# Performance work log

Measured on AMD Instinct MI355X. Metric: run time of the kernel, lower is better.

## Reference

```python
import jax, jax.numpy as jnp
import numpy as np

GEOM_W = 0.01
N_ITERS = 5
HUBER_DELTA = 1.345
LM_EPS = 1e-6


def _skew(w):
    x, y, z = w[..., 0], w[..., 1], w[..., 2]
    o = jnp.zeros_like(x)
    return jnp.stack([
        jnp.stack([o, -z, y], -1),
        jnp.stack([z, o, -x], -1),
        jnp.stack([-y, x, o], -1)], -2)


def _se3_exp(xi):
    # xi: [B,6] = (v, w), translation first (matches Jt = [I | -skew(X)])
    v, w = xi[..., :3], xi[..., 3:]
    t2 = jnp.sum(w * w, -1)[..., None, None]
    small = t2 < 1e-8
    t2s = jnp.where(small, 1.0, t2)
    th = jnp.sqrt(t2s)
    A = jnp.where(small, 1.0 - t2 / 6.0, jnp.sin(th) / th)
    Bc = jnp.where(small, 0.5 - t2 / 24.0, (1.0 - jnp.cos(th)) / t2s)
    Cc = jnp.where(small, 1.0 / 6.0 - t2 / 120.0, (th - jnp.sin(th)) / (t2s * th))
    wx = _skew(w)
    wx2 = jnp.matmul(wx, wx)
    I3 = jnp.eye(3, dtype=xi.dtype)
    R = I3 + A * wx + Bc * wx2
    V = I3 + Bc * wx + Cc * wx2
    t = jnp.einsum('bij,bj->bi', V, v)
    top = jnp.concatenate([R, t[..., None]], -1)           # [B,3,4]
    bot = jnp.broadcast_to(jnp.array([0.0, 0.0, 0.0, 1.0], dtype=xi.dtype), top[..., :1, :].shape)
    return jnp.concatenate([top, bot], -2)                 # [B,4,4]


def _grid_sample(img, gx, gy):
    # bilinear, padding_mode='zeros', align_corners=True; img [B,C,H,W], gx/gy [B,H,W] in [-1,1]
    B, C, H, W = img.shape
    x = (gx + 1.0) * 0.5 * (W - 1)
    y = (gy + 1.0) * 0.5 * (H - 1)
    x0 = jnp.floor(x)
    y0 = jnp.floor(y)
    fx1 = x - x0
    fy1 = y - y0
    flat = img.reshape(B, C, H * W)

    def corner(xi, yi, wgt):
        inb = (xi >= 0) & (xi <= W - 1) & (yi >= 0) & (yi <= H - 1)
        xc = jnp.clip(xi, 0, W - 1).astype(jnp.int32)
        yc = jnp.clip(yi, 0, H - 1).astype(jnp.int32)
        idx = (yc * W + xc).reshape(B, 1, H * W)
        vals = jnp.take_along_axis(flat, idx, axis=2).reshape(B, C, H, W)
        return vals * (wgt * inb)[:, None]

    return (corner(x0, y0, (1 - fx1) * (1 - fy1)) + corner(x0 + 1, y0, fx1 * (1 - fy1))
            + corner(x0, y0 + 1, (1 - fx1) * fy1) + corner(x0 + 1, y0 + 1, fx1 * fy1))


def _feature_gradient(img):
    # central differences with replicate padding: [B,C,H,W] -> (d/dx, d/dy)
    px = jnp.pad(img, ((0, 0), (0, 0), (0, 0), (1, 1)), mode='edge')
    py = jnp.pad(img, ((0, 0), (0, 0), (1, 1), (0, 0)), mode='edge')
    dx = 0.5 * (px[..., 2:] - px[..., :-2])
    dy = 0.5 * (py[..., 2:, :] - py[..., :-2, :])
    return dx, dy


def _forward(pose, I0, I1, invD0, invD1, intrinsics, depth0, depth1):
    B, C, H, W = I0.shape
    dt = I0.dtype
    fxv = intrinsics[:, 0][:, None, None]
    fyv = intrinsics[:, 1][:, None, None]
    cx = intrinsics[:, 2][:, None, None]
    cy = intrinsics[:, 3][:, None, None]
    vv, uu = jnp.meshgrid(jnp.arange(H, dtype=dt), jnp.arange(W, dtype=dt), indexing='ij')
    d1 = depth1[:, 0]
    # back-projected points in frame 1: [B,H,W,3]
    X1 = jnp.stack([d1 * (uu - cx) / fxv, d1 * (vv - cy) / fyv, d1], -1)
    dI0x, dI0y = _feature_gradient(I0)
    dD0x, dD0y = _feature_gradient(depth0)
    eye3 = jnp.eye(3, dtype=dt)
    lam = GEOM_W
    for _ in range(N_ITERS):
        R = pose[:, :3, :3]
        t = pose[:, :3, 3]
        X0 = jnp.einsum('bij,bhwj->bhwi', R, X1) + t[:, None, None, :]   # [B,H,W,3]
        x, y, z = X0[..., 0], X0[..., 1], X0[..., 2]
        vproj = z > 1e-6
        zs = jnp.where(vproj, z, 1.0)
        u0 = fxv * x / zs + cx
        v0 = fyv * y / zs + cy
        d = z
        inb = (u0 > 0) & (u0 < W - 1) & (v0 > 0) & (v0 < H - 1)
        valid = inb & vproj & (depth0[:, 0] > 0) & (depth1[:, 0] > 0)    # [B,H,W]
        zero = jnp.zeros_like(zs)
        row0 = jnp.stack([fxv / zs + zero, zero, -fxv * x / (zs * zs)], -1)
        row1 = jnp.stack([zero, fyv / zs + zero, -fyv * y / (zs * zs)], -1)
        Jp = jnp.stack([row0, row1], -2)                                  # [B,H,W,2,3]
        Jt = jnp.concatenate([jnp.broadcast_to(eye3, (B, H, W, 3, 3)), -_skew(X0)], -1)  # [B,H,W,3,6]
        Jw = jnp.einsum('bhwij,bhwjk->bhwik', Jp, Jt)                     # [B,H,W,2,6]
        gx = jnp.clip((u0 / (W - 1) - 0.5) * 2.0, -2.0, 2.0)
        gy = jnp.clip((v0 / (H - 1) - 0.5) * 2.0, -2.0, 2.0)
        I0w = _grid_sample(I0, gx, gy)
        r_I = I1 - I0w                                                    # [B,C,H,W]
        D0w = _grid_sample(depth0, gx, gy)
        r_Z = d[:, None] - D0w                                            # [B,1,H,W]
        gI = jnp.stack([_grid_sample(dI0x, gx, gy), _grid_sample(dI0y, gx, gy)], -1)  # [B,C,H,W,2]
        J_I = jnp.einsum('bchwn,bhwnk->bchwk', gI, Jw)                    # [B,C,H,W,6]
        gD = jnp.stack([_grid_sample(dD0x, gx, gy), _grid_sample(dD0y, gx, gy)], -1)  # [B,1,H,W,2]
        J_Z = jnp.einsum('bchwn,bhwnk->bchwk', gD, Jw) - Jt[..., 2, :][:, None]       # [B,1,H,W,6]
        vexp = jnp.broadcast_to(valid[:, None], (B, C + 1, H, W)).reshape(B, -1).astype(dt)
        J = jnp.concatenate([J_I.reshape(B, -1, 6), lam * J_Z.reshape(B, -1, 6)], 1) * vexp[..., None]
        r = jnp.concatenate([r_I.reshape(B, -1), lam * r_Z.reshape(B, -1)], 1) * vexp
        ar = jnp.abs(r)
        wts = jnp.where(ar <= HUBER_DELTA, 1.0, HUBER_DELTA / jnp.maximum(ar, 1e-8))  # Huber M-estimator
        JtJ = jnp.einsum('bnk,bnl->bkl', J, wts[..., None] * J)           # [B,6,6]
        Hs = JtJ + LM_EPS * jnp.eye(6, dtype=dt)                          # LM damping
        Rhs = jnp.einsum('bnk,bn->bk', J, wts * r)                        # [B,6]
        xi = jnp.linalg.solve(Hs, Rhs[..., None])[..., 0]                 # batched 6x6 solve
        pose = jnp.matmul(_se3_exp(xi), pose)                             # left-multiplicative retraction
    return pose


def setup_inputs() -> dict:
    key = jax.random.key(0)
    ks = jax.random.split(key, 5)
    B, C, H, W = 4, 16, 240, 320
    I0 = jax.random.normal(ks[0], (B, C, H, W), jnp.float32)
    I1 = jax.random.normal(ks[1], (B, C, H, W), jnp.float32)
    depth0 = jax.random.uniform(ks[2], (B, 1, H, W), jnp.float32, 0.5, 2.0)
    depth1 = jax.random.uniform(ks[3], (B, 1, H, W), jnp.float32, 0.5, 2.0)
    invD0 = 1.0 / depth0
    invD1 = 1.0 / depth1
    intrinsics = jnp.tile(jnp.array([[250.0, 250.0, (W - 1) / 2.0, (H - 1) / 2.0]], jnp.float32), (B, 1))
    xi0 = 0.01 * jax.random.normal(ks[4], (B, 6), jnp.float32)
    pose = _se3_exp(xi0)
    return {'pose': pose, 'I0': I0, 'I1': I1, 'invD0': invD0, 'invD1': invD1,
            'intrinsics': intrinsics, 'depth0': depth0, 'depth1': depth1}


def reference(pose, I0, I1, invD0, invD1, intrinsics, depth0, depth1):
    return _forward(pose, I0, I1, invD0, invD1, intrinsics, depth0, depth1)
```

## Files before the change

### kernel.cpp

```cpp
#include <hip/hip_runtime.h>
#include <math.h>

#define B_   4
#define C_   16
#define H_   240
#define W_   320
#define HW_  (H_*W_)
#define NPB  128
#define NBLK (HW_/NPB)
#define NACC 27
#define GEOM_W_ 0.01f
#define HUBER_  1.345f
#define LM_EPS_ 1e-6
#define N_ITERS_ 5

__global__ void dia_init(const float* __restrict__ pose_in, float* __restrict__ pose,
                         double* __restrict__ acc) {
    const int i = threadIdx.x;
    if (i < N_ITERS_ * B_ * NACC) acc[i] = 0.0;
    if (i < B_ * 16) pose[i] = pose_in[i];
}

__device__ __forceinline__ void samp12(const float* __restrict__ img,
                                       int x0, int y0, int xm1, int xp2, int ym1, int yp2,
                                       float w00, float w10, float w01, float w11,
                                       float& sv, float& sdx, float& sdy)
{
    const float* r0 = img + y0 * W_;
    const float* r1 = r0 + W_;
    float A0 = r0[xm1], A1 = r0[x0], A2 = r0[x0+1], A3 = r0[xp2];
    float B0 = r1[xm1], B1 = r1[x0], B2 = r1[x0+1], B3 = r1[xp2];
    const float* ru = img + ym1 * W_;
    const float* rd = img + yp2 * W_;
    float U0 = ru[x0], U1 = ru[x0+1];
    float D0 = rd[x0], D1 = rd[x0+1];
    sv  = w00*A1 + w10*A2 + w01*B1 + w11*B2;
    sdx = 0.5f*( w00*(A2-A0) + w10*(A3-A1) + w01*(B2-B0) + w11*(B3-B1) );
    sdy = 0.5f*( w00*(B1-U0) + w10*(B2-U1) + w01*(D0-A1) + w11*(D1-A2) );
}

__global__ __launch_bounds__(256, 6) void dia_reduce(
    const float* __restrict__ pose,
    const float* __restrict__ I0,
    const float* __restrict__ I1,
    const float* __restrict__ intr,
    const float* __restrict__ depth0,
    const float* __restrict__ depth1,
    double* __restrict__ acc)
{
    const int b    = blockIdx.y;
    const int half = threadIdx.x >> 7;
    const int lp   = threadIdx.x & 127;
    const int p    = blockIdx.x * NPB + lp;

    const float fxv = intr[b*4+0], fyv = intr[b*4+1];
    const float cx  = intr[b*4+2], cy  = intr[b*4+3];
    const float ifx = 1.0f / fxv,  ify = 1.0f / fyv;

    float Rm[9], tv[3];
#pragma unroll
    for (int i = 0; i < 3; ++i) {
#pragma unroll
        for (int j = 0; j < 3; ++j) Rm[i*3+j] = pose[b*16 + i*4 + j];
        tv[i] = pose[b*16 + i*4 + 3];
    }

    const float* d0p = depth0 + b * HW_;
    const float* d1p = depth1 + b * HW_;
    const float* I0b = I0 + (size_t)b * C_ * HW_ + (size_t)(half * 8) * HW_;
    const float* I1b = I1 + (size_t)b * C_ * HW_ + (size_t)(half * 8) * HW_;

    float c27[NACC];
#pragma unroll
    for (int i = 0; i < NACC; ++i) c27[i] = 0.f;

    {
        const int v = p / W_;
        const int u = p - v * W_;

        const float d1 = d1p[p];
        const float d0 = d0p[p];
        const float X1x = d1 * ((float)u - cx) * ifx;
        const float X1y = d1 * ((float)v - cy) * ify;
        const float x = Rm[0]*X1x + Rm[1]*X1y + Rm[2]*d1 + tv[0];
        const float y = Rm[3]*X1x + Rm[4]*X1y + Rm[5]*d1 + tv[1];
        const float z = Rm[6]*X1x + Rm[7]*X1y + Rm[8]*d1 + tv[2];

        const bool vproj = z > 1e-6f;
        const float zs = vproj ? z : 1.0f;
        const float iz = 1.0f / zs;
        const float u0 = fxv * x * iz + cx;
        const float v0 = fyv * y * iz + cy;
        const bool inb = (u0 > 0.f) && (u0 < (float)(W_-1)) && (v0 > 0.f) && (v0 < (float)(H_-1));
        const bool valid = inb && vproj && (d0 > 0.f) && (d1 > 0.f);

        if (valid) {
            const float x0f = floorf(u0), y0f = floorf(v0);
            const int x0 = (int)x0f, y0 = (int)y0f;
            const float fx1 = u0 - x0f, fy1 = v0 - y0f;
            const float w00 = (1.f-fx1)*(1.f-fy1), w10 = fx1*(1.f-fy1);
            const float w01 = (1.f-fx1)*fy1,       w11 = fx1*fy1;
            const int xm1 = max(x0-1, 0), xp2 = min(x0+2, W_-1);
            const int ym1 = max(y0-1, 0), yp2 = min(y0+2, H_-1);

            float Jw[2][6];
            {
                const float a0 = fxv * iz;
                const float a2 = -fxv * x * iz * iz;
                const float b1 = fyv * iz;
                const float b2 = -fyv * y * iz * iz;
                Jw[0][0] = a0;        Jw[0][1] = 0.f;      Jw[0][2] = a2;
                Jw[0][3] = a2 * y;    Jw[0][4] = a0*z - a2*x; Jw[0][5] = -a0*y;
                Jw[1][0] = 0.f;       Jw[1][1] = b1;       Jw[1][2] = b2;
                Jw[1][3] = -b1*z + b2*y; Jw[1][4] = -b2*x; Jw[1][5] = b1*x;
            }

            float JZ[6] = {0.f,0.f,0.f,0.f,0.f,0.f};
            float wz2 = 0.f, rZ = 0.f;
            if (half == 0) {
                float D0w, dDx, dDy;
                samp12(d0p, x0, y0, xm1, xp2, ym1, yp2, w00, w10, w01, w11, D0w, dDx, dDy);
                rZ = z - D0w;
                JZ[0] = dDx*Jw[0][0] + dDy*Jw[1][0];
                JZ[1] = dDx*Jw[0][1] + dDy*Jw[1][1];
                JZ[2] = dDx*Jw[0][2] + dDy*Jw[1][2] - 1.f;
                JZ[3] = dDx*Jw[0][3] + dDy*Jw[1][3] - y;
                JZ[4] = dDx*Jw[0][4] + dDy*Jw[1][4] + x;
                JZ[5] = dDx*Jw[0][5] + dDy*Jw[1][5];
                const float arz = fabsf(GEOM_W_ * rZ);
                const float wzw = (arz <= HUBER_) ? 1.f : HUBER_ / fmaxf(arz, 1e-8f);
                wz2 = wzw * GEOM_W_ * GEOM_W_;
            }

            float Ga = 0.f, Gb = 0.f, Gd = 0.f, grx = 0.f, gry = 0.f;
            for (int c = 0; c < 8; ++c) {
                const float* ip = I0b + c * HW_;
                float Iw, gxc, gyc;
                samp12(ip, x0, y0, xm1, xp2, ym1, yp2, w00, w10, w01, w11, Iw, gxc, gyc);
                const float r = I1b[c * HW_ + p] - Iw;
                const float ar = fabsf(r);
                const float wc = (ar <= HUBER_) ? 1.f : HUBER_ / fmaxf(ar, 1e-8f);
                Ga  += wc * gxc * gxc;
                Gb  += wc * gxc * gyc;
                Gd  += wc * gyc * gyc;
                grx += wc * r * gxc;
                gry += wc * r * gyc;
            }

            int k = 0;
#pragma unroll
            for (int i = 0; i < 6; ++i) {
#pragma unroll
                for (int j = i; j < 6; ++j) {
                    c27[k++] = Ga * Jw[0][i] * Jw[0][j]
                             + Gb * (Jw[0][i] * Jw[1][j] + Jw[1][i] * Jw[0][j])
                             + Gd * Jw[1][i] * Jw[1][j]
                             + wz2 * JZ[i] * JZ[j];
                }
            }
#pragma unroll
            for (int i = 0; i < 6; ++i)
                c27[21 + i] = grx * Jw[0][i] + gry * Jw[1][i] + wz2 * rZ * JZ[i];
        }
    }

    __shared__ float sred[4][NACC];
    const int lane = threadIdx.x & 63;
    const int wid  = threadIdx.x >> 6;
#pragma unroll
    for (int i = 0; i < NACC; ++i) {
        float vs = c27[i];
#pragma unroll
        for (int off = 32; off > 0; off >>= 1) vs += __shfl_down(vs, off, 64);
        if (lane == 0) sred[wid][i] = vs;
    }
    __syncthreads();
    if (threadIdx.x < NACC) {
        const double s = (double)sred[0][threadIdx.x] + (double)sred[1][threadIdx.x]
                       + (double)sred[2][threadIdx.x] + (double)sred[3][threadIdx.x];
        atomicAdd(&acc[b * NACC + threadIdx.x], s);
    }
}

__global__ __launch_bounds__(128) void dia_solve(const double* __restrict__ acc,
                                                 float* __restrict__ pose)
{
    __shared__ double S[B_][NACC];
    const int t = threadIdx.x;
    if (t < B_ * NACC) {
        const int b = t / NACC, i = t - b * NACC;
        S[b][i] = acc[b * NACC + i];
    }
    __syncthreads();
    if (t < B_) {
        double Hm[6][7];
        {
            double JtJ[6][6];
            int k = 0;
            for (int i = 0; i < 6; ++i)
                for (int j = i; j < 6; ++j) { JtJ[i][j] = S[t][k]; JtJ[j][i] = S[t][k]; ++k; }
            for (int i = 0; i < 6; ++i) {
                for (int j = 0; j < 6; ++j) Hm[i][j] = JtJ[i][j] + (i == j ? LM_EPS_ : 0.0);
                Hm[i][6] = S[t][21 + i];
            }
        }
        double xi[6];
        for (int col = 0; col < 6; ++col) {
            int piv = col; double mx = fabs(Hm[col][col]);
            for (int r2 = col+1; r2 < 6; ++r2) { double a = fabs(Hm[r2][col]); if (a > mx) { mx = a; piv = r2; } }
            if (piv != col)
                for (int j2 = col; j2 < 7; ++j2) { double tmp = Hm[col][j2]; Hm[col][j2] = Hm[piv][j2]; Hm[piv][j2] = tmp; }
            const double inv = 1.0 / Hm[col][col];
            for (int r2 = col+1; r2 < 6; ++r2) {
                const double f = Hm[r2][col] * inv;
                for (int j2 = col; j2 < 7; ++j2) Hm[r2][j2] -= f * Hm[col][j2];
            }
        }
        for (int r2 = 5; r2 >= 0; --r2) {
            double s = Hm[r2][6];
            for (int j2 = r2+1; j2 < 6; ++j2) s -= Hm[r2][j2] * xi[j2];
            xi[r2] = s / Hm[r2][r2];
        }

        const double vx = xi[0], vy = xi[1], vz = xi[2];
        const double wx = xi[3], wy = xi[4], wz = xi[5];
        const double t2 = wx*wx + wy*wy + wz*wz;
        double A, Bc, Cc;
        if (t2 < 1e-8) {
            A  = 1.0 - t2 / 6.0;
            Bc = 0.5 - t2 / 24.0;
            Cc = 1.0/6.0 - t2 / 120.0;
        } else {
            const double th = sqrt(t2);
            const double sth = sin(th), cth = cos(th);
            A  = sth / th;
            Bc = (1.0 - cth) / t2;
            Cc = (th - sth) / (t2 * th);
        }
        const double Wm[9]  = { 0.0, -wz,  wy,
                                wz,  0.0, -wx,
                               -wy,  wx,  0.0 };
        double W2[9];
        for (int i = 0; i < 3; ++i)
            for (int j = 0; j < 3; ++j) {
                double s = 0.0;
                for (int k = 0; k < 3; ++k) s += Wm[i*3+k] * Wm[k*3+j];
                W2[i*3+j] = s;
            }
        double Rm[9], Vm[9];
        for (int i = 0; i < 9; ++i) {
            const double id = (i % 4 == 0) ? 1.0 : 0.0;
            Rm[i] = id + A  * Wm[i] + Bc * W2[i];
            Vm[i] = id + Bc * Wm[i] + Cc * W2[i];
        }
        const double tx = Vm[0]*vx + Vm[1]*vy + Vm[2]*vz;
        const double ty = Vm[3]*vx + Vm[4]*vy + Vm[5]*vz;
        const double tz = Vm[6]*vx + Vm[7]*vy + Vm[8]*vz;

        float* P = pose + t * 16;
        double Pm[16];
        for (int i = 0; i < 16; ++i) Pm[i] = (double)P[i];
        double E[16] = { Rm[0], Rm[1], Rm[2], tx,
                         Rm[3], Rm[4], Rm[5], ty,
                         Rm[6], Rm[7], Rm[8], tz,
                         0.0,   0.0,   0.0,   1.0 };
        double out[16];
        for (int i = 0; i < 4; ++i)
            for (int j = 0; j < 4; ++j) {
                double s = 0.0;
                for (int k = 0; k < 4; ++k) s += E[i*4+k] * Pm[k*4+j];
                out[i*4+j] = s;
            }
        for (int i = 0; i < 16; ++i) P[i] = (float)out[i];
    }
}

extern "C" void kernel_launch(void* const* d_in, const int* in_sizes, int n_in,
                              void* d_out, int out_size, void* d_ws, size_t ws_size,
                              hipStream_t stream) {
    const float* pose_in = (const float*)d_in[0];
    const float* I0      = (const float*)d_in[1];
    const float* I1      = (const float*)d_in[2];
    const float* intr    = (const float*)d_in[5];
    const float* depth0  = (const float*)d_in[6];
    const float* depth1  = (const float*)d_in[7];

    float*  pose = (float*)d_out;
    double* acc  = (double*)d_ws;

    hipLaunchKernelGGL(dia_init, dim3(1), dim3(576), 0, stream, pose_in, pose, acc);
    for (int it = 0; it < N_ITERS_; ++it) {
        double* acc_it = acc + (size_t)it * B_ * NACC;
        hipLaunchKernelGGL(dia_reduce, dim3(NBLK, B_), dim3(256), 0, stream,
                           pose, I0, I1, intr, depth0, depth1, acc_it);
        hipLaunchKernelGGL(dia_solve, dim3(1), dim3(128), 0, stream, acc_it, pose);
    }
}
```

Measured before the change: 451.6 us.

## Fuse solve into reduce via last-block ticket and widen per-thread channel loop

The per-iteration solve kernel is removed. The last block to finish for each batch element, detected with an atomic ticket counter, now solves the 6x6 system and updates the pose. Each thread now handles one pixel across all 16 channels instead of splitting channels between two half-blocks, which halves the block count and drops the duplicated geometry work. Image taps use vectorized 4-wide and 2-wide loads on interior pixels, and the 27 accumulator values are computed right at reduction time to lower register pressure. The trade-offs are a serial solve tail inside the last block and fewer threads in flight per pixel.

```diff
diff --git a/kernel.cpp b/kernel.cpp
--- a/kernel.cpp
+++ b/kernel.cpp
@@ -6,52 +6,145 @@
 #define H_   240
 #define W_   320
 #define HW_  (H_*W_)
-#define NPB  128
-#define NBLK (HW_/NPB)
+#define TPB  256
+#define NBLK (HW_/TPB)
 #define NACC 27
 #define GEOM_W_ 0.01f
 #define HUBER_  1.345f
 #define LM_EPS_ 1e-6
 #define N_ITERS_ 5
 
+typedef float f4u __attribute__((ext_vector_type(4), aligned(4)));
+typedef float f2u __attribute__((ext_vector_type(2), aligned(4)));
+
 __global__ void dia_init(const float* __restrict__ pose_in, float* __restrict__ pose,
-                         double* __restrict__ acc) {
+                         double* __restrict__ acc, int* __restrict__ tick) {
     const int i = threadIdx.x;
     if (i < N_ITERS_ * B_ * NACC) acc[i] = 0.0;
+    if (i < N_ITERS_ * B_) tick[i] = 0;
     if (i < B_ * 16) pose[i] = pose_in[i];
 }
 
-__device__ __forceinline__ void samp12(const float* __restrict__ img,
-                                       int x0, int y0, int xm1, int xp2, int ym1, int yp2,
-                                       float w00, float w10, float w01, float w11,
-                                       float& sv, float& sdx, float& sdy)
+__device__ __forceinline__ void samp12v(const float* __restrict__ base,
+                                        int x0, bool interior, int xm1, int xp2,
+                                        int ro0, int rum, int rdp,
+                                        float w00, float w10, float w01, float w11,
+                                        float& sv, float& sdx, float& sdy)
 {
-    const float* r0 = img + y0 * W_;
+    const float* r0 = base + ro0;
     const float* r1 = r0 + W_;
-    float A0 = r0[xm1], A1 = r0[x0], A2 = r0[x0+1], A3 = r0[xp2];
-    float B0 = r1[xm1], B1 = r1[x0], B2 = r1[x0+1], B3 = r1[xp2];
-    const float* ru = img + ym1 * W_;
-    const float* rd = img + yp2 * W_;
-    float U0 = ru[x0], U1 = ru[x0+1];
-    float D0 = rd[x0], D1 = rd[x0+1];
+    float A0, A1, A2, A3, B0, B1, B2, B3;
+    if (interior) {
+        f4u a = *(const f4u*)(r0 + x0 - 1);
+        f4u c = *(const f4u*)(r1 + x0 - 1);
+        A0 = a[0]; A1 = a[1]; A2 = a[2]; A3 = a[3];
+        B0 = c[0]; B1 = c[1]; B2 = c[2]; B3 = c[3];
+    } else {
+        A0 = r0[xm1]; A1 = r0[x0]; A2 = r0[x0+1]; A3 = r0[xp2];
+        B0 = r1[xm1]; B1 = r1[x0]; B2 = r1[x0+1]; B3 = r1[xp2];
+    }
+    f2u uv = *(const f2u*)(base + rum + x0);
+    f2u dv = *(const f2u*)(base + rdp + x0);
     sv  = w00*A1 + w10*A2 + w01*B1 + w11*B2;
     sdx = 0.5f*( w00*(A2-A0) + w10*(A3-A1) + w01*(B2-B0) + w11*(B3-B1) );
-    sdy = 0.5f*( w00*(B1-U0) + w10*(B2-U1) + w01*(D0-A1) + w11*(D1-A2) );
-}
-
-__global__ __launch_bounds__(256, 6) void dia_reduce(
-    const float* __restrict__ pose,
+    sdy = 0.5f*( w00*(B1-uv[0]) + w10*(B2-uv[1]) + w01*(dv[0]-A1) + w11*(dv[1]-A2) );
+}
+
+__device__ __attribute__((noinline)) void solve_update(const double* __restrict__ S,
+                                                       float* __restrict__ P)
+{
+    double Hm[6][7];
+    {
+        int k = 0;
+        double JtJ[6][6];
+        for (int i = 0; i < 6; ++i)
+            for (int j = i; j < 6; ++j) { JtJ[i][j] = S[k]; JtJ[j][i] = S[k]; ++k; }
+        for (int i = 0; i < 6; ++i) {
+            for (int j = 0; j < 6; ++j) Hm[i][j] = JtJ[i][j] + (i == j ? LM_EPS_ : 0.0);
+            Hm[i][6] = S[21 + i];
+        }
+    }
+    double xi[6];
+    for (int col = 0; col < 6; ++col) {
+        int piv = col; double mx = fabs(Hm[col][col]);
+        for (int r2 = col+1; r2 < 6; ++r2) { double a = fabs(Hm[r2][col]); if (a > mx) { mx = a; piv = r2; } }
+        if (piv != col)
+            for (int j2 = col; j2 < 7; ++j2) { double tmp = Hm[col][j2]; Hm[col][j2] = Hm[piv][j2]; Hm[piv][j2] = tmp; }
+        const double inv = 1.0 / Hm[col][col];
+        for (int r2 = col+1; r2 < 6; ++r2) {
+            const double f = Hm[r2][col] * inv;
+            for (int j2 = col; j2 < 7; ++j2) Hm[r2][j2] -= f * Hm[col][j2];
+        }
+    }
+    for (int r2 = 5; r2 >= 0; --r2) {
+        double s = Hm[r2][6];
+        for (int j2 = r2+1; j2 < 6; ++j2) s -= Hm[r2][j2] * xi[j2];
+        xi[r2] = s / Hm[r2][r2];
+    }
+
+    const double vx = xi[0], vy = xi[1], vz = xi[2];
+    const double wx = xi[3], wy = xi[4], wz = xi[5];
+    const double t2 = wx*wx + wy*wy + wz*wz;
+    double A, Bc, Cc;
+    if (t2 < 1e-8) {
+        A  = 1.0 - t2 / 6.0;
+        Bc = 0.5 - t2 / 24.0;
+        Cc = 1.0/6.0 - t2 / 120.0;
+    } else {
+        const double th = sqrt(t2);
+        const double sth = sin(th), cth = cos(th);
+        A  = sth / th;
+        Bc = (1.0 - cth) / t2;
+        Cc = (th - sth) / (t2 * th);
+    }
+    const double Wm[9] = { 0.0, -wz,  wy,
+                           wz,  0.0, -wx,
+                          -wy,  wx,  0.0 };
+    double W2[9];
+    for (int i = 0; i < 3; ++i)
+        for (int j = 0; j < 3; ++j) {
+            double s = 0.0;
+            for (int k = 0; k < 3; ++k) s += Wm[i*3+k] * Wm[k*3+j];
+            W2[i*3+j] = s;
+        }
+    double Rm[9], Vm[9];
+    for (int i = 0; i < 9; ++i) {
+        const double id = (i % 4 == 0) ? 1.0 : 0.0;
+        Rm[i] = id + A  * Wm[i] + Bc * W2[i];
+        Vm[i] = id + Bc * Wm[i] + Cc * W2[i];
+    }
+    const double tx = Vm[0]*vx + Vm[1]*vy + Vm[2]*vz;
+    const double ty = Vm[3]*vx + Vm[4]*vy + Vm[5]*vz;
+    const double tz = Vm[6]*vx + Vm[7]*vy + Vm[8]*vz;
+
+    double Pm[16];
+    for (int i = 0; i < 16; ++i) Pm[i] = (double)P[i];
+    double E[16] = { Rm[0], Rm[1], Rm[2], tx,
+                     Rm[3], Rm[4], Rm[5], ty,
+                     Rm[6], Rm[7], Rm[8], tz,
+                     0.0,   0.0,   0.0,   1.0 };
+    double out[16];
+    for (int i = 0; i < 4; ++i)
+        for (int j = 0; j < 4; ++j) {
+            double s = 0.0;
+            for (int k = 0; k < 4; ++k) s += E[i*4+k] * Pm[k*4+j];
+            out[i*4+j] = s;
+        }
+    for (int i = 0; i < 16; ++i) P[i] = (float)out[i];
+}
+
+__global__ __launch_bounds__(256, 5) void dia_reduce(
+    float* __restrict__ pose,
     const float* __restrict__ I0,
     const float* __restrict__ I1,
     const float* __restrict__ intr,
     const float* __restrict__ depth0,
     const float* __restrict__ depth1,
-    double* __restrict__ acc)
+    double* __restrict__ acc,
+    int* __restrict__ tick)
 {
-    const int b    = blockIdx.y;
-    const int half = threadIdx.x >> 7;
-    const int lp   = threadIdx.x & 127;
-    const int p    = blockIdx.x * NPB + lp;
+    const int b = blockIdx.y;
+    const int p = blockIdx.x * TPB + threadIdx.x;
 
     const float fxv = intr[b*4+0], fyv = intr[b*4+1];
     const float cx  = intr[b*4+2], cy  = intr[b*4+3];
@@ -67,12 +160,13 @@
 
     const float* d0p = depth0 + b * HW_;
     const float* d1p = depth1 + b * HW_;
-    const float* I0b = I0 + (size_t)b * C_ * HW_ + (size_t)(half * 8) * HW_;
-    const float* I1b = I1 + (size_t)b * C_ * HW_ + (size_t)(half * 8) * HW_;
-
-    float c27[NACC];
-#pragma unroll
-    for (int i = 0; i < NACC; ++i) c27[i] = 0.f;
+    const float* I0b = I0 + (size_t)b * C_ * HW_;
+    const float* I1b = I1 + (size_t)b * C_ * HW_;
+
+    float Jw0[6] = {0,0,0,0,0,0};
+    float Jw1[6] = {0,0,0,0,0,0};
+    float JZ[6]  = {0,0,0,0,0,0};
+    float Ga = 0.f, Gb = 0.f, Gd = 0.f, grx = 0.f, gry = 0.f, wz2 = 0.f, rZ = 0.f;
 
     {
         const int v = p / W_;
@@ -102,42 +196,41 @@
             const float w01 = (1.f-fx1)*fy1,       w11 = fx1*fy1;
             const int xm1 = max(x0-1, 0), xp2 = min(x0+2, W_-1);
             const int ym1 = max(y0-1, 0), yp2 = min(y0+2, H_-1);
-
-            float Jw[2][6];
+            const bool interior = (x0 >= 1) && (x0 <= W_-3);
+            const int ro0 = y0 * W_;
+            const int rum = ym1 * W_;
+            const int rdp = yp2 * W_;
+
             {
                 const float a0 = fxv * iz;
                 const float a2 = -fxv * x * iz * iz;
                 const float b1 = fyv * iz;
                 const float b2 = -fyv * y * iz * iz;
-                Jw[0][0] = a0;        Jw[0][1] = 0.f;      Jw[0][2] = a2;
-                Jw[0][3] = a2 * y;    Jw[0][4] = a0*z - a2*x; Jw[0][5] = -a0*y;
-                Jw[1][0] = 0.f;       Jw[1][1] = b1;       Jw[1][2] = b2;
-                Jw[1][3] = -b1*z + b2*y; Jw[1][4] = -b2*x; Jw[1][5] = b1*x;
+                Jw0[0] = a0;           Jw0[1] = 0.f;   Jw0[2] = a2;
+                Jw0[3] = a2 * y;       Jw0[4] = a0*z - a2*x; Jw0[5] = -a0*y;
+                Jw1[0] = 0.f;          Jw1[1] = b1;    Jw1[2] = b2;
+                Jw1[3] = -b1*z + b2*y; Jw1[4] = -b2*x; Jw1[5] = b1*x;
             }
 
-            float JZ[6] = {0.f,0.f,0.f,0.f,0.f,0.f};
-            float wz2 = 0.f, rZ = 0.f;
-            if (half == 0) {
+            {
                 float D0w, dDx, dDy;
-                samp12(d0p, x0, y0, xm1, xp2, ym1, yp2, w00, w10, w01, w11, D0w, dDx, dDy);
+                samp12v(d0p, x0, interior, xm1, xp2, ro0, rum, rdp,
+                        w00, w10, w01, w11, D0w, dDx, dDy);
                 rZ = z - D0w;
-                JZ[0] = dDx*Jw[0][0] + dDy*Jw[1][0];
-                JZ[1] = dDx*Jw[0][1] + dDy*Jw[1][1];
-                JZ[2] = dDx*Jw[0][2] + dDy*Jw[1][2] - 1.f;
-                JZ[3] = dDx*Jw[0][3] + dDy*Jw[1][3] - y;
-                JZ[4] = dDx*Jw[0][4] + dDy*Jw[1][4] + x;
-                JZ[5] = dDx*Jw[0][5] + dDy*Jw[1][5];
+#pragma unroll
+                for (int j = 0; j < 6; ++j) JZ[j] = dDx*Jw0[j] + dDy*Jw1[j];
+                JZ[2] -= 1.f; JZ[3] -= y; JZ[4] += x;
                 const float arz = fabsf(GEOM_W_ * rZ);
                 const float wzw = (arz <= HUBER_) ? 1.f : HUBER_ / fmaxf(arz, 1e-8f);
                 wz2 = wzw * GEOM_W_ * GEOM_W_;
             }
 
-            float Ga = 0.f, Gb = 0.f, Gd = 0.f, grx = 0.f, gry = 0.f;
-            for (int c = 0; c < 8; ++c) {
-                const float* ip = I0b + c * HW_;
+#pragma unroll 2
+            for (int c = 0; c < C_; ++c) {
                 float Iw, gxc, gyc;
-                samp12(ip, x0, y0, xm1, xp2, ym1, yp2, w00, w10, w01, w11, Iw, gxc, gyc);
-                const float r = I1b[c * HW_ + p] - Iw;
+                samp12v(I0b + (size_t)c * HW_, x0, interior, xm1, xp2, ro0, rum, rdp,
+                        w00, w10, w01, w11, Iw, gxc, gyc);
+                const float r = I1b[(size_t)c * HW_ + p] - Iw;
                 const float ar = fabsf(r);
                 const float wc = (ar <= HUBER_) ? 1.f : HUBER_ / fmaxf(ar, 1e-8f);
                 Ga  += wc * gxc * gxc;
@@ -146,33 +239,33 @@
                 grx += wc * r * gxc;
                 gry += wc * r * gyc;
             }
-
-            int k = 0;
-#pragma unroll
-            for (int i = 0; i < 6; ++i) {
-#pragma unroll
-                for (int j = i; j < 6; ++j) {
-                    c27[k++] = Ga * Jw[0][i] * Jw[0][j]
-                             + Gb * (Jw[0][i] * Jw[1][j] + Jw[1][i] * Jw[0][j])
-                             + Gd * Jw[1][i] * Jw[1][j]
-                             + wz2 * JZ[i] * JZ[j];
-                }
-            }
-#pragma unroll
-            for (int i = 0; i < 6; ++i)
-                c27[21 + i] = grx * Jw[0][i] + gry * Jw[1][i] + wz2 * rZ * JZ[i];
         }
     }
 
     __shared__ float sred[4][NACC];
     const int lane = threadIdx.x & 63;
     const int wid  = threadIdx.x >> 6;
-#pragma unroll
-    for (int i = 0; i < NACC; ++i) {
-        float vs = c27[i];
-#pragma unroll
-        for (int off = 32; off > 0; off >>= 1) vs += __shfl_down(vs, off, 64);
-        if (lane == 0) sred[wid][i] = vs;
+    int k = 0;
+#pragma unroll
+    for (int i = 0; i < 6; ++i) {
+#pragma unroll
+        for (int j = i; j < 6; ++j) {
+            float vt = Ga * Jw0[i] * Jw0[j]
+                     + Gb * (Jw0[i] * Jw1[j] + Jw1[i] * Jw0[j])
+                     + Gd * Jw1[i] * Jw1[j]
+                     + wz2 * JZ[i] * JZ[j];
+#pragma unroll
+            for (int off = 32; off > 0; off >>= 1) vt += __shfl_down(vt, off, 64);
+            if (lane == 0) sred[wid][k] = vt;
+            ++k;
+        }
+    }
+#pragma unroll
+    for (int i = 0; i < 6; ++i) {
+        float vt = grx * Jw0[i] + gry * Jw1[i] + wz2 * rZ * JZ[i];
+#pragma unroll
+        for (int off = 32; off > 0; off >>= 1) vt += __shfl_down(vt, off, 64);
+        if (lane == 0) sred[wid][21 + i] = vt;
     }
     __syncthreads();
     if (threadIdx.x < NACC) {
@@ -180,98 +273,18 @@
                        + (double)sred[2][threadIdx.x] + (double)sred[3][threadIdx.x];
         atomicAdd(&acc[b * NACC + threadIdx.x], s);
     }
-}
-
-__global__ __launch_bounds__(128) void dia_solve(const double* __restrict__ acc,
-                                                 float* __restrict__ pose)
-{
-    __shared__ double S[B_][NACC];
-    const int t = threadIdx.x;
-    if (t < B_ * NACC) {
-        const int b = t / NACC, i = t - b * NACC;
-        S[b][i] = acc[b * NACC + i];
-    }
     __syncthreads();
-    if (t < B_) {
-        double Hm[6][7];
-        {
-            double JtJ[6][6];
-            int k = 0;
-            for (int i = 0; i < 6; ++i)
-                for (int j = i; j < 6; ++j) { JtJ[i][j] = S[t][k]; JtJ[j][i] = S[t][k]; ++k; }
-            for (int i = 0; i < 6; ++i) {
-                for (int j = 0; j < 6; ++j) Hm[i][j] = JtJ[i][j] + (i == j ? LM_EPS_ : 0.0);
-                Hm[i][6] = S[t][21 + i];
-            }
-        }
-        double xi[6];
-        for (int col = 0; col < 6; ++col) {
-            int piv = col; double mx = fabs(Hm[col][col]);
-            for (int r2 = col+1; r2 < 6; ++r2) { double a = fabs(Hm[r2][col]); if (a > mx) { mx = a; piv = r2; } }
-            if (piv != col)
-                for (int j2 = col; j2 < 7; ++j2) { double tmp = Hm[col][j2]; Hm[col][j2] = Hm[piv][j2]; Hm[piv][j2] = tmp; }
-            const double inv = 1.0 / Hm[col][col];
-            for (int r2 = col+1; r2 < 6; ++r2) {
-                const double f = Hm[r2][col] * inv;
-                for (int j2 = col; j2 < 7; ++j2) Hm[r2][j2] -= f * Hm[col][j2];
-            }
-        }
-        for (int r2 = 5; r2 >= 0; --r2) {
-            double s = Hm[r2][6];
-            for (int j2 = r2+1; j2 < 6; ++j2) s -= Hm[r2][j2] * xi[j2];
-            xi[r2] = s / Hm[r2][r2];
-        }
-
-        const double vx = xi[0], vy = xi[1], vz = xi[2];
-        const double wx = xi[3], wy = xi[4], wz = xi[5];
-        const double t2 = wx*wx + wy*wy + wz*wz;
-        double A, Bc, Cc;
-        if (t2 < 1e-8) {
-            A  = 1.0 - t2 / 6.0;
-            Bc = 0.5 - t2 / 24.0;
-            Cc = 1.0/6.0 - t2 / 120.0;
-        } else {
-            const double th = sqrt(t2);
-            const double sth = sin(th), cth = cos(th);
-            A  = sth / th;
-            Bc = (1.0 - cth) / t2;
-            Cc = (th - sth) / (t2 * th);
-        }
-        const double Wm[9]  = { 0.0, -wz,  wy,
-                                wz,  0.0, -wx,
-                               -wy,  wx,  0.0 };
-        double W2[9];
-        for (int i = 0; i < 3; ++i)
-            for (int j = 0; j < 3; ++j) {
-                double s = 0.0;
-                for (int k = 0; k < 3; ++k) s += Wm[i*3+k] * Wm[k*3+j];
-                W2[i*3+j] = s;
-            }
-        double Rm[9], Vm[9];
-        for (int i = 0; i < 9; ++i) {
-            const double id = (i % 4 == 0) ? 1.0 : 0.0;
-            Rm[i] = id + A  * Wm[i] + Bc * W2[i];
-            Vm[i] = id + Bc * Wm[i] + Cc * W2[i];
-        }
-        const double tx = Vm[0]*vx + Vm[1]*vy + Vm[2]*vz;
-        const double ty = Vm[3]*vx + Vm[4]*vy + Vm[5]*vz;
-        const double tz = Vm[6]*vx + Vm[7]*vy + Vm[8]*vz;
-
-        float* P = pose + t * 16;
-        double Pm[16];
-        for (int i = 0; i < 16; ++i) Pm[i] = (double)P[i];
-        double E[16] = { Rm[0], Rm[1], Rm[2], tx,
-                         Rm[3], Rm[4], Rm[5], ty,
-                         Rm[6], Rm[7], Rm[8], tz,
-                         0.0,   0.0,   0.0,   1.0 };
-        double out[16];
-        for (int i = 0; i < 4; ++i)
-            for (int j = 0; j < 4; ++j) {
-                double s = 0.0;
-                for (int k = 0; k < 4; ++k) s += E[i*4+k] * Pm[k*4+j];
-                out[i*4+j] = s;
-            }
-        for (int i = 0; i < 16; ++i) P[i] = (float)out[i];
+
+    if (threadIdx.x == 0) {
+        __threadfence();
+        const int old = atomicAdd(&tick[b], 1);
+        if (old == NBLK - 1) {
+            __threadfence();
+            double S[NACC];
+            for (int i = 0; i < NACC; ++i)
+                S[i] = atomicAdd(&acc[b * NACC + i], 0.0);
+            solve_update(S, pose + b * 16);
+        }
     }
 }
 
@@ -287,12 +300,12 @@
 
     float*  pose = (float*)d_out;
     double* acc  = (double*)d_ws;
-
-    hipLaunchKernelGGL(dia_init, dim3(1), dim3(576), 0, stream, pose_in, pose, acc);
+    int*    tick = (int*)(acc + N_ITERS_ * B_ * NACC);
+
+    hipLaunchKernelGGL(dia_init, dim3(1), dim3(576), 0, stream, pose_in, pose, acc, tick);
     for (int it = 0; it < N_ITERS_; ++it) {
-        double* acc_it = acc + (size_t)it * B_ * NACC;
-        hipLaunchKernelGGL(dia_reduce, dim3(NBLK, B_), dim3(256), 0, stream,
-                           pose, I0, I1, intr, depth0, depth1, acc_it);
-        hipLaunchKernelGGL(dia_solve, dim3(1), dim3(128), 0, stream, acc_it, pose);
-    }
-}
+        hipLaunchKernelGGL(dia_reduce, dim3(NBLK, B_), dim3(TPB), 0, stream,
+                           pose, I0, I1, intr, depth0, depth1,
+                           acc + (size_t)it * B_ * NACC, tick + (size_t)it * B_);
+    }
+}
```

New measurement: 433.6 us. 4.0% less time.
